# Performance work log

Hardware: AMD Instinct MI355X
Metric: run time of the kernel (lower is better)

Reference implementation:

```python
import jax, jax.numpy as jnp
import numpy as np

B, T, D = 1, 8192, 1024
H, DH = 16, 64
WIN = 128          # attention window (tokens on each side)
WB = 128
NB = T // WB
EPS = 1e-5


def _layernorm(x, g, b):
    mu = jnp.mean(x, axis=-1, keepdims=True)
    var = jnp.mean(jnp.square(x - mu), axis=-1, keepdims=True)
    return (x - mu) * jax.lax.rsqrt(var + EPS) * g + b


def _band_mask():
    # query offset i in [0, WB), key offset j in [0, 3*WB) within [prev|self|next] blocks
    i = jnp.arange(WB)[:, None]
    j = jnp.arange(3 * WB)[None, :]
    rel = j - WB - i                      # key_pos - query_pos
    band = jnp.abs(rel) <= WIN            # sliding window |i-j| <= W (matches torch mask)
    blk = jnp.arange(NB)[:, None, None]
    key_pos = blk * WB + (j - WB)[None]   # absolute key position
    return band[None] & (key_pos >= 0) & (key_pos < T)   # [NB, WB, 3*WB]


def _local_attention(q, k, v):
    # q,k,v: [B,H,T,DH] -> block-local SDPA, mathematically identical to
    # full SDPA with the additive band mask in the torch code.
    def blocks(t):
        return t.reshape(B, H, NB, WB, DH)
    qb = blocks(q)
    kp = jnp.pad(blocks(k), ((0, 0), (0, 0), (1, 1), (0, 0), (0, 0)))
    vp = jnp.pad(blocks(v), ((0, 0), (0, 0), (1, 1), (0, 0), (0, 0)))
    # gather [prev, self, next] key/value blocks: [B,H,NB,3*WB,DH]
    k3 = jnp.concatenate([kp[:, :, s:s + NB] for s in range(3)], axis=3)
    v3 = jnp.concatenate([vp[:, :, s:s + NB] for s in range(3)], axis=3)
    scores = jnp.einsum('bhnqd,bhnkd->bhnqk', qb, k3) / np.sqrt(DH).astype(np.float32)
    mask = _band_mask()                                   # [NB,WB,3WB]
    scores = jnp.where(mask[None, None], scores, -jnp.inf)
    attn = jax.nn.softmax(scores, axis=-1)
    out = jnp.einsum('bhnqk,bhnkd->bhnqd', attn, v3)      # [B,H,NB,WB,DH]
    return out.reshape(B, H, T, DH)


def setup_inputs() -> dict:
    key = jax.random.key(0)
    ks = jax.random.split(key, 7)
    s = 0.02
    return {
        'x': jax.random.normal(ks[0], (B, T, D), jnp.float32),
        'wq': jax.random.normal(ks[1], (D, D), jnp.float32) * s,
        'wk': jax.random.normal(ks[2], (D, D), jnp.float32) * s,
        'wv': jax.random.normal(ks[3], (D, D), jnp.float32) * s,
        'wo': jax.random.normal(ks[4], (D, D), jnp.float32) * s,
        'wg': jax.random.normal(ks[5], (D, 2 * D), jnp.float32) * s,
        'wd': jax.random.normal(ks[6], (2 * D, D), jnp.float32) * s,
        'norm_g': jnp.ones((D,), jnp.float32),
        'norm_b': jnp.zeros((D,), jnp.float32),
        'ffn_g': jnp.ones((D,), jnp.float32),
        'ffn_b': jnp.zeros((D,), jnp.float32),
    }


def reference(x, wq, wk, wv, wo, wg, wd, norm_g, norm_b, ffn_g, ffn_b):
    h = _layernorm(x, norm_g, norm_b)
    def heads(t):  # [B,T,D] -> [B,H,T,DH]
        return t.reshape(B, T, H, DH).transpose(0, 2, 1, 3)
    q, k, v = heads(h @ wq), heads(h @ wk), heads(h @ wv)
    attn_out = _local_attention(q, k, v)                     # [B,H,T,DH]
    attn_out = attn_out.transpose(0, 2, 1, 3).reshape(B, T, D)
    x = x + attn_out @ wo
    h = _layernorm(x, ffn_g, ffn_b)
    x = x + jax.nn.silu(h @ wg) @ wd
    return x
```

## Files before the change

kernel.cpp:

```cpp
#include <hip/hip_runtime.h>
#include <cstdint>

#define T_DIM 8192
#define D_DIM 1024
#define NB_DIM 64
#define QKS 2048

typedef __bf16 bf16x8 __attribute__((ext_vector_type(8)));
typedef __bf16 bf16x4 __attribute__((ext_vector_type(4)));
typedef float f32x4 __attribute__((ext_vector_type(4)));

#define MFMA16(a, b, c) __builtin_amdgcn_mfma_f32_16x16x32_bf16((a), (b), (c), 0, 0, 0)
#define BAR() asm volatile("s_barrier" ::: "memory")
#define LGK0()                                          \
  asm volatile("s_waitcnt lgkmcnt(0)" ::: "memory");    \
  __builtin_amdgcn_sched_barrier(0)
#define VMCNT(n) asm volatile("s_waitcnt vmcnt(" #n ")" ::: "memory")

__device__ __forceinline__ void gld_lds16(const void* gsrc, void* ldst) {
  __builtin_amdgcn_global_load_lds(
      (__attribute__((address_space(1))) void*)(uintptr_t)gsrc,
      (__attribute__((address_space(3))) void*)(uintptr_t)ldst,
      16, 0, 0);
}

__global__ __launch_bounds__(256) void transpose_cvt(
    const float* __restrict__ W, __bf16* __restrict__ Wt, int K, int N) {
  __shared__ float tile[32][33];
  const int tx = threadIdx.x & 31, ty = threadIdx.x >> 5;
  const int n0 = blockIdx.x * 32, k0 = blockIdx.y * 32;
#pragma unroll
  for (int i = 0; i < 32; i += 8)
    tile[ty + i][tx] = W[(size_t)(k0 + ty + i) * N + n0 + tx];
  __syncthreads();
#pragma unroll
  for (int i = 0; i < 32; i += 8)
    Wt[(size_t)(n0 + ty + i) * K + k0 + tx] = (__bf16)tile[tx][ty + i];
}

template <typename TI>
__global__ __launch_bounds__(256) void ln_kernel(
    const TI* __restrict__ x, const float* __restrict__ g,
    const float* __restrict__ b, __bf16* __restrict__ out) {
  __shared__ float red[8];
  const int row = blockIdx.x, tid = threadIdx.x;
  float v0, v1, v2, v3;
  if constexpr (sizeof(TI) == 4) {
    const float4 v = ((const float4*)(x + (size_t)row * D_DIM))[tid];
    v0 = v.x; v1 = v.y; v2 = v.z; v3 = v.w;
  } else {
    const bf16x4 v = ((const bf16x4*)(x + (size_t)row * D_DIM))[tid];
    v0 = (float)v[0]; v1 = (float)v[1]; v2 = (float)v[2]; v3 = (float)v[3];
  }
  float s = v0 + v1 + v2 + v3;
#pragma unroll
  for (int off = 32; off >= 1; off >>= 1) s += __shfl_xor(s, off, 64);
  if ((tid & 63) == 0) red[tid >> 6] = s;
  __syncthreads();
  const float mean = (red[0] + red[1] + red[2] + red[3]) * (1.0f / D_DIM);
  const float d0 = v0 - mean, d1 = v1 - mean, d2 = v2 - mean, d3 = v3 - mean;
  float ss = d0 * d0 + d1 * d1 + d2 * d2 + d3 * d3;
#pragma unroll
  for (int off = 32; off >= 1; off >>= 1) ss += __shfl_xor(ss, off, 64);
  if ((tid & 63) == 0) red[4 + (tid >> 6)] = ss;
  __syncthreads();
  const float var = (red[4] + red[5] + red[6] + red[7]) * (1.0f / D_DIM);
  const float rstd = rsqrtf(var + 1e-5f);
  const float4 gg = ((const float4*)g)[tid];
  const float4 bb = ((const float4*)b)[tid];
  bf16x4 o;
  o[0] = (__bf16)(d0 * rstd * gg.x + bb.x);
  o[1] = (__bf16)(d1 * rstd * gg.y + bb.y);
  o[2] = (__bf16)(d2 * rstd * gg.z + bb.z);
  o[3] = (__bf16)(d3 * rstd * gg.w + bb.w);
  *(bf16x4*)(out + (size_t)row * D_DIM + tid * 4) = o;
}

__global__ __launch_bounds__(256, 2) void gemm_vt(
    const __bf16* __restrict__ A, const __bf16* __restrict__ Bt,
    __bf16* __restrict__ Cout, int M, int N, int K) {
  __shared__ __bf16 smem[32768];
  __bf16* As = smem;
  __bf16* Bs = smem + 16384;
  const int tid = threadIdx.x;
  const int l = tid & 63, w = tid >> 6;
  const int lr = l & 15, lg = l >> 4;
  const int wr = w >> 1, wc = w & 1;
  const int bm = blockIdx.y, bn = blockIdx.x;
  const size_t arow0 = (size_t)bm * 128;
  const size_t brow0 = (size_t)bn * 128;

  f32x4 acc[4][4];
  const f32x4 z4 = {0.f, 0.f, 0.f, 0.f};
#pragma unroll
  for (int m = 0; m < 4; ++m)
#pragma unroll
    for (int n = 0; n < 4; ++n) acc[m][n] = z4;

  auto stage = [&](int buf, int k0) {
#pragma unroll
    for (int r = 0; r < 4; ++r) {
      int ci = r * 256 + tid;
      int row = ci >> 3, c8 = ci & 7;
      gld_lds16(A + (arow0 + row) * K + k0 + c8 * 8, &As[buf * 8192 + ci * 8]);
    }
#pragma unroll
    for (int r = 0; r < 4; ++r) {
      int ci = r * 256 + tid;
      int row = ci >> 3, c8 = ci & 7;
      gld_lds16(Bt + (brow0 + row) * K + k0 + c8 * 8, &Bs[buf * 8192 + ci * 8]);
    }
  };

  stage(0, 0);
  const int nk = K >> 6;
  int cur = 0;
  __syncthreads();

  for (int t = 0; t < nk; ++t) {
    if (t + 1 < nk) stage(cur ^ 1, (t + 1) << 6);
#pragma unroll
    for (int kk = 0; kk < 2; ++kk) {
      bf16x8 af[4], bf_[4];
#pragma unroll
      for (int m = 0; m < 4; ++m)
        af[m] = *(const bf16x8*)&As[cur * 8192 + (wr * 64 + m * 16 + lr) * 64 + kk * 32 + lg * 8];
#pragma unroll
      for (int n = 0; n < 4; ++n)
        bf_[n] = *(const bf16x8*)&Bs[cur * 8192 + (wc * 64 + n * 16 + lr) * 64 + kk * 32 + lg * 8];
#pragma unroll
      for (int m = 0; m < 4; ++m)
#pragma unroll
        for (int n = 0; n < 4; ++n) acc[m][n] = MFMA16(af[m], bf_[n], acc[m][n]);
    }
    __syncthreads();
    cur ^= 1;
  }

  __bf16* Tt = smem;
#pragma unroll
  for (int m = 0; m < 4; ++m)
#pragma unroll
    for (int n = 0; n < 4; ++n)
#pragma unroll
      for (int r = 0; r < 4; ++r)
        Tt[(wc * 64 + n * 16 + lr) * 136 + wr * 64 + m * 16 + lg * 4 + r] =
            (__bf16)acc[m][n][r];
  __syncthreads();
#pragma unroll
  for (int i = 0; i < 8; ++i) {
    const int ci = i * 256 + tid;
    const int c = ci >> 4;
    const int rr = (ci & 15) * 8;
    const bf16x8 vv = *(const bf16x8*)&Tt[c * 136 + rr];
    *(bf16x8*)(Cout + (size_t)(bn * 128 + c) * M + bm * 128 + rr) = vv;
  }
}

template <int BM_, int EPI>
__global__ __launch_bounds__(512, 2) void gemm8(
    const __bf16* __restrict__ A, const __bf16* __restrict__ Bt,
    const void* __restrict__ Res, void* __restrict__ Cout,
    int M, int N, int K, int nbn) {
  constexpr int MF = BM_ / 32;
  constexpr int MH = MF / 2;
  constexpr int SA = 8 * MF;
  constexpr int LA = BM_ / 128;
  constexpr int ATILE = BM_ * 64;
  constexpr int AHALF = BM_ * 32;
  constexpr int BOFF = 2 * ATILE;
  __shared__ __bf16 lds[2 * BM_ * 64 + 32768];

  const int tid = threadIdx.x;
  const int l = tid & 63, w = tid >> 6;
  const int lr = l & 15, lg = l >> 4;
  const int wr = w >> 2, wc = w & 3;
  const int nwg = gridDim.x;
  const int bid = (int)blockIdx.x;
  const int swz = (bid & 7) * (nwg >> 3) + (bid >> 3);
  const int bm = swz / nbn, bn = swz % nbn;
  const int am0 = bm * BM_, bn0 = bn * 256;

  f32x4 acc[MF][4];
  const f32x4 z4 = {0.f, 0.f, 0.f, 0.f};
#pragma unroll
  for (int m = 0; m < MF; ++m)
#pragma unroll
    for (int n = 0; n < 4; ++n) acc[m][n] = z4;

  auto stageA = [&](int h, int b, int k0) {
#pragma unroll
    for (int r = 0; r < LA; ++r) {
      const int ci = r * 512 + tid;
      const int wri = ci >> 3, c8 = ci & 7;
      const int ra = (wri % SA) + (wri / SA) * (2 * SA) + h * SA;
      gld_lds16(A + (size_t)(am0 + ra) * K + k0 + ((c8 ^ (wri & 7)) << 3),
                (__bf16*)lds + b * ATILE + h * AHALF + ci * 8);
    }
  };
  auto stageB = [&](int h, int b, int k0) {
#pragma unroll
    for (int r = 0; r < 2; ++r) {
      const int ci = r * 512 + tid;
      const int wri = ci >> 3, c8 = ci & 7;
      const int rb = (wri & 31) + (wri >> 5) * 64 + h * 32;
      gld_lds16(Bt + (size_t)(bn0 + rb) * K + k0 + ((c8 ^ (wri & 7)) << 3),
                (__bf16*)lds + BOFF + b * 16384 + h * 8192 + ci * 8);
    }
  };

  int buf = 0;
  auto lda = [&](int mh, int i, int kk) -> bf16x8 {
    const int rl = (i * 16 + lr) + wr * SA;
    const int ch = (kk * 4 + lg) ^ (rl & 7);
    return *(const bf16x8*)&lds[buf * ATILE + mh * AHALF + rl * 64 + ch * 8];
  };
  auto ldb = [&](int nh, int j, int kk) -> bf16x8 {
    const int rl = (j * 16 + lr) + wc * 32;
    const int ch = (kk * 4 + lg) ^ (rl & 7);
    return *(const bf16x8*)&lds[BOFF + buf * 16384 + nh * 8192 + rl * 64 + ch * 8];
  };

  const int nt = K >> 6;
  stageA(0, 0, 0);
  stageB(1, 0, 0);
  stageB(0, 0, 0);
  stageA(1, 0, 0);
  stageA(0, 1, 64);
  stageB(1, 1, 64);
  if constexpr (BM_ == 256) VMCNT(6); else VMCNT(4);
  BAR();

  bf16x8 afr[MH][2], bfr[2][2];
  for (int t = 0; t < nt; ++t) {
    const bool s1 = (t + 1 < nt);
    const bool s2 = (t + 2 < nt);
    const int b1 = (t + 1) & 1;
    const int k1 = (t + 1) << 6;
    const int k2 = (t + 2) << 6;

#pragma unroll
    for (int i = 0; i < MH; ++i)
#pragma unroll
      for (int kk = 0; kk < 2; ++kk) afr[i][kk] = lda(0, i, kk);
#pragma unroll
    for (int j = 0; j < 2; ++j)
#pragma unroll
      for (int kk = 0; kk < 2; ++kk) bfr[j][kk] = ldb(0, j, kk);
    if (s1) stageB(0, b1, k1);
    BAR();
    LGK0();
    __builtin_amdgcn_s_setprio(1);
#pragma unroll
    for (int i = 0; i < MH; ++i)
#pragma unroll
      for (int j = 0; j < 2; ++j)
#pragma unroll
        for (int kk = 0; kk < 2; ++kk)
          acc[i][j] = MFMA16(afr[i][kk], bfr[j][kk], acc[i][j]);
    __builtin_amdgcn_sched_barrier(0);
    __builtin_amdgcn_s_setprio(0);
    BAR();

#pragma unroll
    for (int j = 0; j < 2; ++j)
#pragma unroll
      for (int kk = 0; kk < 2; ++kk) bfr[j][kk] = ldb(1, j, kk);
    if (s1) {
      stageA(1, b1, k1);
      if constexpr (BM_ == 256) VMCNT(8); else VMCNT(6);
    }
    BAR();
    LGK0();
    __builtin_amdgcn_s_setprio(1);
#pragma unroll
    for (int i = 0; i < MH; ++i)
#pragma unroll
      for (int j = 0; j < 2; ++j)
#pragma unroll
        for (int kk = 0; kk < 2; ++kk)
          acc[i][2 + j] = MFMA16(afr[i][kk], bfr[j][kk], acc[i][2 + j]);
    __builtin_amdgcn_sched_barrier(0);
    __builtin_amdgcn_s_setprio(0);
    BAR();

#pragma unroll
    for (int i = 0; i < MH; ++i)
#pragma unroll
      for (int kk = 0; kk < 2; ++kk) afr[i][kk] = lda(1, i, kk);
    if (s2) stageA(0, buf, k2);
    BAR();
    LGK0();
    __builtin_amdgcn_s_setprio(1);
#pragma unroll
    for (int i = 0; i < MH; ++i)
#pragma unroll
      for (int j = 0; j < 2; ++j)
#pragma unroll
        for (int kk = 0; kk < 2; ++kk)
          acc[MH + i][2 + j] = MFMA16(afr[i][kk], bfr[j][kk], acc[MH + i][2 + j]);
    __builtin_amdgcn_sched_barrier(0);
    __builtin_amdgcn_s_setprio(0);
    BAR();

#pragma unroll
    for (int j = 0; j < 2; ++j)
#pragma unroll
      for (int kk = 0; kk < 2; ++kk) bfr[j][kk] = ldb(0, j, kk);
    if (s2) {
      stageB(1, buf, k2);
      if constexpr (BM_ == 256) VMCNT(6); else VMCNT(4);
    } else if (s1) {
      VMCNT(0);
    }
    BAR();
    LGK0();
    __builtin_amdgcn_s_setprio(1);
#pragma unroll
    for (int i = 0; i < MH; ++i)
#pragma unroll
      for (int j = 0; j < 2; ++j)
#pragma unroll
        for (int kk = 0; kk < 2; ++kk)
          acc[MH + i][j] = MFMA16(afr[i][kk], bfr[j][kk], acc[MH + i][j]);
    __builtin_amdgcn_sched_barrier(0);
    __builtin_amdgcn_s_setprio(0);
    BAR();

    buf ^= 1;
  }

  if constexpr (EPI == 5) {
    const __bf16* R = (const __bf16*)Res;
    float* O = (float*)Cout;
#pragma unroll
    for (int mf = 0; mf < MF; ++mf)
#pragma unroll
      for (int nf = 0; nf < 4; ++nf)
#pragma unroll
        for (int r = 0; r < 4; ++r) {
          const int row = am0 + wr * 2 * SA + mf * 16 + lg * 4 + r;
          const int col = bn0 + wc * 64 + nf * 16 + lr;
          const size_t idx = (size_t)row * N + col;
          O[idx] = acc[mf][nf][r] + (float)R[idx];
        }
  } else {
    __bf16* Ct = (__bf16*)lds;
#pragma unroll
    for (int mf = 0; mf < MF; ++mf)
#pragma unroll
      for (int nf = 0; nf < 4; ++nf)
#pragma unroll
        for (int r = 0; r < 4; ++r) {
          const int rl = wr * 2 * SA + mf * 16 + lg * 4 + r;
          const int cl = wc * 64 + nf * 16 + lr;
          float v = acc[mf][nf][r];
          if constexpr (EPI == 3) v = v / (1.f + __expf(-v));
          if constexpr (EPI == 4)
            v += ((const float*)Res)[(size_t)(am0 + rl) * N + bn0 + cl];
          Ct[rl * 256 + cl] = (__bf16)v;
        }
    __syncthreads();
    __bf16* O = (__bf16*)Cout;
#pragma unroll
    for (int i = 0; i < BM_ / 16; ++i) {
      const int ci = i * 512 + tid;
      const int row = ci >> 5, c8 = ci & 31;
      *(bf16x8*)(O + (size_t)(am0 + row) * N + bn0 + c8 * 8) =
          *(const bf16x8*)&Ct[row * 256 + c8 * 8];
    }
  }
}

__global__ __launch_bounds__(256, 2) void attn_kernel(
    const __bf16* __restrict__ qk, const __bf16* __restrict__ vT,
    __bf16* __restrict__ out) {
  __shared__ __bf16 Pl[4][32 * 136];

  const int tid = threadIdx.x;
  const int l = tid & 63, w = tid >> 6;
  const int lr = l & 15, lg = l >> 4;
  const int bx = (int)blockIdx.x;
  const int swz = (bx & 7) * 128 + (bx >> 3);
  const int h = swz >> 6;
  const int blk = swz & 63;
  __bf16* Pw = Pl[w];

  const __bf16* qbase =
      qk + (size_t)(blk * 128 + w * 32 + lr) * QKS + h * 64 + lg * 8;
  bf16x8 qf[2][2];
#pragma unroll
  for (int m = 0; m < 2; ++m)
#pragma unroll
    for (int ks = 0; ks < 2; ++ks)
      qf[m][ks] = *(const bf16x8*)(qbase + (size_t)m * 16 * QKS + ks * 32);

  const f32x4 z4 = {0.f, 0.f, 0.f, 0.f};
  float ssum[2][4];
  f32x4 o[2][4];
#pragma unroll
  for (int m = 0; m < 2; ++m) {
#pragma unroll
    for (int r = 0; r < 4; ++r) ssum[m][r] = 0.f;
#pragma unroll
    for (int n = 0; n < 4; ++n) o[m][n] = z4;
  }

  for (int it = 0; it < 3; ++it) {
    const int kb = blk + it - 1;
    if (kb < 0 || kb >= NB_DIM) continue;
    const int rel = it - 1;
    const int kclo = (rel < 0) ? (w * 2) : 0;
    const int kchi = (rel > 0) ? (w * 2 + 2) : 8;

    f32x4 s[2][8];
    const __bf16* kbase =
        qk + (size_t)(kb * 128 + lr) * QKS + 1024 + h * 64 + lg * 8;
#pragma unroll
    for (int kc = 0; kc < 8; ++kc) {
      if (kc < kclo || kc >= kchi) continue;
      const bf16x8 k0 = *(const bf16x8*)(kbase + (size_t)kc * 16 * QKS);
      const bf16x8 k1 = *(const bf16x8*)(kbase + (size_t)kc * 16 * QKS + 32);
      s[0][kc] = MFMA16(qf[0][0], k0, z4);
      s[1][kc] = MFMA16(qf[1][0], k0, z4);
      s[0][kc] = MFMA16(qf[0][1], k1, s[0][kc]);
      s[1][kc] = MFMA16(qf[1][1], k1, s[1][kc]);
    }

#pragma unroll
    for (int m = 0; m < 2; ++m) {
#pragma unroll
      for (int r = 0; r < 4; ++r) {
        const int qi = w * 32 + m * 16 + lg * 4 + r;
        float acc_s = 0.f;
#pragma unroll
        for (int kc = 0; kc < 8; ++kc) {
          if (kc < kclo || kc >= kchi) continue;
          const int kj = kc * 16 + lr;
          float p = __expf(s[m][kc][r] * 0.125f);
          const bool valid = (rel == 0) || (rel < 0 ? (kj >= qi) : (kj <= qi));
          p = valid ? p : 0.f;
          s[m][kc][r] = p;
          acc_s += p;
        }
        ssum[m][r] += acc_s;
      }
    }

#pragma unroll
    for (int m = 0; m < 2; ++m)
#pragma unroll
      for (int kc = 0; kc < 8; ++kc) {
        if (kc < kclo || kc >= kchi) continue;
#pragma unroll
        for (int r = 0; r < 4; ++r)
          Pw[(m * 16 + lg * 4 + r) * 136 + kc * 16 + lr] = (__bf16)s[m][kc][r];
      }

    const int kslo = kclo >> 1, kshi = kchi >> 1;
    const __bf16* vbase =
        vT + (size_t)(h * 64 + lr) * T_DIM + kb * 128 + lg * 8;
#pragma unroll
    for (int ks = 0; ks < 4; ++ks) {
      if (ks < kslo || ks >= kshi) continue;
      bf16x8 pa[2];
#pragma unroll
      for (int m = 0; m < 2; ++m)
        pa[m] = *(const bf16x8*)&Pw[(m * 16 + lr) * 136 + ks * 32 + lg * 8];
#pragma unroll
      for (int n = 0; n < 4; ++n) {
        const bf16x8 vb = *(const bf16x8*)(vbase + (size_t)n * 16 * T_DIM + ks * 32);
        o[0][n] = MFMA16(pa[0], vb, o[0][n]);
        o[1][n] = MFMA16(pa[1], vb, o[1][n]);
      }
    }
  }

  float inv[2][4];
#pragma unroll
  for (int m = 0; m < 2; ++m)
#pragma unroll
    for (int r = 0; r < 4; ++r) {
      float rs = ssum[m][r];
#pragma unroll
      for (int off = 1; off < 16; off <<= 1) rs += __shfl_xor(rs, off, 64);
      inv[m][r] = __builtin_amdgcn_rcpf(rs);
    }
#pragma unroll
  for (int m = 0; m < 2; ++m)
#pragma unroll
    for (int n = 0; n < 4; ++n)
#pragma unroll
      for (int r = 0; r < 4; ++r)
        Pw[(m * 16 + lg * 4 + r) * 136 + n * 16 + lr] =
            (__bf16)(o[m][n][r] * inv[m][r]);
#pragma unroll
  for (int i = 0; i < 4; ++i) {
    const int ci = i * 64 + l;
    const int qrow = ci >> 3;
    const int c8 = (ci & 7) * 8;
    const bf16x8 vv = *(const bf16x8*)&Pw[qrow * 136 + c8];
    *(bf16x8*)(out + (size_t)(blk * 128 + w * 32 + qrow) * D_DIM + h * 64 + c8) = vv;
  }
}

extern "C" void kernel_launch(void* const* d_in, const int* in_sizes, int n_in,
                              void* d_out, int out_size, void* d_ws, size_t ws_size,
                              hipStream_t stream) {
  (void)in_sizes; (void)n_in; (void)out_size; (void)ws_size;
  const float* x      = (const float*)d_in[0];
  const float* wq     = (const float*)d_in[1];
  const float* wk     = (const float*)d_in[2];
  const float* wv     = (const float*)d_in[3];
  const float* wo     = (const float*)d_in[4];
  const float* wg     = (const float*)d_in[5];
  const float* wd     = (const float*)d_in[6];
  const float* norm_g = (const float*)d_in[7];
  const float* norm_b = (const float*)d_in[8];
  const float* ffn_g  = (const float*)d_in[9];
  const float* ffn_b  = (const float*)d_in[10];
  float* out = (float*)d_out;

  char* ws = (char*)d_ws;
  constexpr size_t MB = 1ull << 20;
  __bf16* wqkT = (__bf16*)(ws + 0 * MB);
  __bf16* wvT  = (__bf16*)(ws + 4 * MB);
  __bf16* woT  = (__bf16*)(ws + 6 * MB);
  __bf16* wgT  = (__bf16*)(ws + 8 * MB);
  __bf16* wdT  = (__bf16*)(ws + 12 * MB);
  __bf16* hbuf = (__bf16*)(ws + 16 * MB);
  __bf16* qkbf = (__bf16*)(ws + 32 * MB);
  __bf16* gbf  = (__bf16*)(ws + 32 * MB);
  __bf16* vTbf = (__bf16*)(ws + 64 * MB);
  __bf16* x2bf = (__bf16*)(ws + 80 * MB);

  transpose_cvt<<<dim3(32, 32), 256, 0, stream>>>(wq, wqkT, 1024, 1024);
  transpose_cvt<<<dim3(32, 32), 256, 0, stream>>>(wk, wqkT + 1024 * 1024, 1024, 1024);
  transpose_cvt<<<dim3(32, 32), 256, 0, stream>>>(wv, wvT, 1024, 1024);
  transpose_cvt<<<dim3(32, 32), 256, 0, stream>>>(wo, woT, 1024, 1024);
  transpose_cvt<<<dim3(64, 32), 256, 0, stream>>>(wg, wgT, 1024, 2048);
  transpose_cvt<<<dim3(32, 64), 256, 0, stream>>>(wd, wdT, 2048, 1024);

  ln_kernel<float><<<8192, 256, 0, stream>>>(x, norm_g, norm_b, hbuf);

  gemm8<256, 0><<<256, 512, 0, stream>>>(hbuf, wqkT, nullptr, qkbf, 8192, 2048, 1024, 8);
  gemm_vt<<<dim3(8, 64), 256, 0, stream>>>(hbuf, wvT, vTbf, 8192, 1024, 1024);

  attn_kernel<<<1024, 256, 0, stream>>>(qkbf, vTbf, hbuf);

  gemm8<128, 4><<<256, 512, 0, stream>>>(hbuf, woT, x, x2bf, 8192, 1024, 1024, 4);

  ln_kernel<__bf16><<<8192, 256, 0, stream>>>(x2bf, ffn_g, ffn_b, hbuf);

  gemm8<256, 3><<<256, 512, 0, stream>>>(hbuf, wgT, nullptr, gbf, 8192, 2048, 1024, 8);

  gemm8<128, 5><<<256, 512, 0, stream>>>(gbf, wdT, x2bf, out, 8192, 1024, 2048, 4);
}
```

Measured before the change: 266.4 us.

## Restructure GEMM main loop to a single-stage prefetch with fewer barriers

Replaces the staggered two-ahead prefetch schedule with a simpler scheme. The whole next K-tile (both A and B halves) is issued early into the alternate buffer, a separate register copy of the B fragments is kept so the last quadrant can reuse them without reloading from LDS, and several barriers plus the sched_barrier fences are removed. The MFMA loops are also reordered so kk is outermost. The aim is to cut LDS reads and synchronisation per iteration. In exchange, prefetch depth drops to one tile, and a VMCNT(0) at the end of each iteration may expose global load latency.

```diff
diff --git a/kernel.cpp b/kernel.cpp
--- a/kernel.cpp
+++ b/kernel.cpp
@@ -223,21 +223,17 @@
 
   const int nt = K >> 6;
   stageA(0, 0, 0);
-  stageB(1, 0, 0);
   stageB(0, 0, 0);
   stageA(1, 0, 0);
-  stageA(0, 1, 64);
-  stageB(1, 1, 64);
-  if constexpr (BM_ == 256) VMCNT(6); else VMCNT(4);
+  stageB(1, 0, 0);
+  VMCNT(0);
   BAR();
 
-  bf16x8 afr[MH][2], bfr[2][2];
+  bf16x8 afr[MH][2], bfr0[2][2], bfr1[2][2];
   for (int t = 0; t < nt; ++t) {
     const bool s1 = (t + 1 < nt);
-    const bool s2 = (t + 2 < nt);
-    const int b1 = (t + 1) & 1;
+    const int nb = buf ^ 1;
     const int k1 = (t + 1) << 6;
-    const int k2 = (t + 2) << 6;
 
 #pragma unroll
     for (int i = 0; i < MH; ++i)
@@ -246,88 +242,73 @@
 #pragma unroll
     for (int j = 0; j < 2; ++j)
 #pragma unroll
-      for (int kk = 0; kk < 2; ++kk) bfr[j][kk] = ldb(0, j, kk);
-    if (s1) stageB(0, b1, k1);
+      for (int kk = 0; kk < 2; ++kk) bfr0[j][kk] = ldb(0, j, kk);
+    if (s1) {
+      stageA(0, nb, k1);
+      stageB(0, nb, k1);
+    }
+    if constexpr (BM_ == 256) asm volatile("s_waitcnt lgkmcnt(8)" ::: "memory");
     BAR();
     LGK0();
     __builtin_amdgcn_s_setprio(1);
 #pragma unroll
-    for (int i = 0; i < MH; ++i)
-#pragma unroll
-      for (int j = 0; j < 2; ++j)
-#pragma unroll
-        for (int kk = 0; kk < 2; ++kk)
-          acc[i][j] = MFMA16(afr[i][kk], bfr[j][kk], acc[i][j]);
-    __builtin_amdgcn_sched_barrier(0);
+    for (int kk = 0; kk < 2; ++kk)
+#pragma unroll
+      for (int i = 0; i < MH; ++i)
+#pragma unroll
+        for (int j = 0; j < 2; ++j)
+          acc[i][j] = MFMA16(afr[i][kk], bfr0[j][kk], acc[i][j]);
     __builtin_amdgcn_s_setprio(0);
-    BAR();
 
 #pragma unroll
     for (int j = 0; j < 2; ++j)
 #pragma unroll
-      for (int kk = 0; kk < 2; ++kk) bfr[j][kk] = ldb(1, j, kk);
+      for (int kk = 0; kk < 2; ++kk) bfr1[j][kk] = ldb(1, j, kk);
     if (s1) {
-      stageA(1, b1, k1);
-      if constexpr (BM_ == 256) VMCNT(8); else VMCNT(6);
+      stageA(1, nb, k1);
+      stageB(1, nb, k1);
     }
     BAR();
     LGK0();
     __builtin_amdgcn_s_setprio(1);
 #pragma unroll
+    for (int kk = 0; kk < 2; ++kk)
+#pragma unroll
+      for (int i = 0; i < MH; ++i)
+#pragma unroll
+        for (int j = 0; j < 2; ++j)
+          acc[i][2 + j] = MFMA16(afr[i][kk], bfr1[j][kk], acc[i][2 + j]);
+    __builtin_amdgcn_s_setprio(0);
+
+#pragma unroll
     for (int i = 0; i < MH; ++i)
 #pragma unroll
-      for (int j = 0; j < 2; ++j)
-#pragma unroll
-        for (int kk = 0; kk < 2; ++kk)
-          acc[i][2 + j] = MFMA16(afr[i][kk], bfr[j][kk], acc[i][2 + j]);
-    __builtin_amdgcn_sched_barrier(0);
-    __builtin_amdgcn_s_setprio(0);
-    BAR();
-
-#pragma unroll
-    for (int i = 0; i < MH; ++i)
-#pragma unroll
       for (int kk = 0; kk < 2; ++kk) afr[i][kk] = lda(1, i, kk);
-    if (s2) stageA(0, buf, k2);
     BAR();
     LGK0();
     __builtin_amdgcn_s_setprio(1);
 #pragma unroll
-    for (int i = 0; i < MH; ++i)
-#pragma unroll
-      for (int j = 0; j < 2; ++j)
-#pragma unroll
-        for (int kk = 0; kk < 2; ++kk)
-          acc[MH + i][2 + j] = MFMA16(afr[i][kk], bfr[j][kk], acc[MH + i][2 + j]);
-    __builtin_amdgcn_sched_barrier(0);
+    for (int kk = 0; kk < 2; ++kk)
+#pragma unroll
+      for (int i = 0; i < MH; ++i)
+#pragma unroll
+        for (int j = 0; j < 2; ++j)
+          acc[MH + i][2 + j] = MFMA16(afr[i][kk], bfr1[j][kk], acc[MH + i][2 + j]);
     __builtin_amdgcn_s_setprio(0);
+
+    if (s1) VMCNT(0);
     BAR();
-
-#pragma unroll
-    for (int j = 0; j < 2; ++j)
-#pragma unroll
-      for (int kk = 0; kk < 2; ++kk) bfr[j][kk] = ldb(0, j, kk);
-    if (s2) {
-      stageB(1, buf, k2);
-      if constexpr (BM_ == 256) VMCNT(6); else VMCNT(4);
-    } else if (s1) {
-      VMCNT(0);
-    }
-    BAR();
-    LGK0();
     __builtin_amdgcn_s_setprio(1);
 #pragma unroll
-    for (int i = 0; i < MH; ++i)
-#pragma unroll
-      for (int j = 0; j < 2; ++j)
-#pragma unroll
-        for (int kk = 0; kk < 2; ++kk)
-          acc[MH + i][j] = MFMA16(afr[i][kk], bfr[j][kk], acc[MH + i][j]);
-    __builtin_amdgcn_sched_barrier(0);
+    for (int kk = 0; kk < 2; ++kk)
+#pragma unroll
+      for (int i = 0; i < MH; ++i)
+#pragma unroll
+        for (int j = 0; j < 2; ++j)
+          acc[MH + i][j] = MFMA16(afr[i][kk], bfr0[j][kk], acc[MH + i][j]);
     __builtin_amdgcn_s_setprio(0);
-    BAR();
-
-    buf ^= 1;
+
+    buf = nb;
   }
 
   if constexpr (EPI == 5) {
@@ -345,6 +326,7 @@
           O[idx] = acc[mf][nf][r] + (float)R[idx];
         }
   } else {
+    __syncthreads();
     __bf16* Ct = (__bf16*)lds;
 #pragma unroll
     for (int mf = 0; mf < MF; ++mf)
```

New measurement: 257.3 us. -3.4%, faster.
